# Kernel tuning notes

Hardware: AMD Instinct MI355X
Metric: run time of the kernel (lower is better)

## Reference

```python
import jax, jax.numpy as jnp
import numpy as np

B, LQ, LKV = 2, 2048, 1024
DQ = DK = DV_IN = 512
H, DQK, DV = 8, 64, 64
DOUT = 512
SPAN, STRIDE = 128, 2


def setup_inputs() -> dict:
    key = jax.random.key(0)
    ks = jax.random.split(key, 7)
    W_SCALE = 0.05  # keep pre-softmax logits in a sane range
    return {
        "q": jax.random.normal(ks[0], (B, LQ, DQ), jnp.float32),
        "k": jax.random.normal(ks[1], (B, LKV, DK), jnp.float32),
        "v": jax.random.normal(ks[2], (B, LKV, DV_IN), jnp.float32),
        "Wq": jax.random.normal(ks[3], (DQ, H * DQK), jnp.float32) * W_SCALE,
        "Wk": jax.random.normal(ks[4], (DK, H * DQK), jnp.float32) * W_SCALE,
        "Wv": jax.random.normal(ks[5], (DV_IN, H * DV), jnp.float32) * W_SCALE,
        "Wout": jax.random.normal(ks[6], (H * DV, DOUT), jnp.float32) * W_SCALE,
        "head_num": H,
        "span": SPAN,
        "stride": STRIDE,
    }


def reference(q, k, v, Wq, Wk, Wv, Wout, head_num, span, stride):
    batch, length_q, _ = q.shape
    length_kv = k.shape[1]
    width = -(-span // stride)  # ceil(span / stride)
    hd_qk = Wq.shape[1] // head_num
    hd_v = Wv.shape[1] // head_num

    Q = (q @ Wq).reshape(batch, length_q, head_num, hd_qk)
    K = (k @ Wk).reshape(batch, length_kv, head_num, hd_qk)
    V = (v @ Wv).reshape(batch, length_kv, head_num, hd_v)

    # Local-window indices: query j attends kv position j//stride + w - (width-1)
    j = jnp.arange(length_q)[:, None]            # [Lq, 1]
    w = jnp.arange(width)[None, :]               # [1, width]
    orig_col = w - (width - 1) + j // stride     # [Lq, width]
    valid = (orig_col >= 0) & (orig_col < length_kv) & \
            ((j % stride) <= span - 1 - (width - w - 1) * stride)
    mask = jnp.where(valid, 0.0, -jnp.inf).astype(q.dtype)
    idx = jnp.clip(orig_col, 0, length_kv - 1)   # masked entries are dont-care

    Kg = K[:, idx]                               # [B, Lq, width, H, dQK]
    # NOTE: original module applies NO 1/sqrt(d) scaling
    scores = jnp.einsum('bjhd,bjwhd->bhjw', Q, Kg) + mask[None, None]
    p = jax.nn.softmax(scores, axis=-1)          # [B, H, Lq, width]

    Vg = V[:, idx]                               # [B, Lq, width, H, dV]
    out = jnp.einsum('bhjw,bjwhd->bjhd', p, Vg)
    out = out.reshape(batch, length_q, head_num * hd_v)
    return out @ Wout
```

## Files before the change

### kernel.cpp

```cpp
#include <hip/hip_runtime.h>
#include <stdint.h>

typedef __bf16 bf16;
typedef __bf16 bf16x8 __attribute__((ext_vector_type(8)));
typedef float f32x4 __attribute__((ext_vector_type(4)));

#define NB    2
#define LQn   2048
#define LKVn  1024
#define DM    512
#define NH    8
#define HD    64

static __device__ __forceinline__ f32x4 mfma_bf16(bf16x8 a, bf16x8 b, f32x4 c) {
  return __builtin_amdgcn_mfma_f32_16x16x32_bf16(a, b, c, 0, 0, 0);
}

__global__ __launch_bounds__(256) void transpose_w_kernel(
    const float* __restrict__ Wq, const float* __restrict__ Wk,
    const float* __restrict__ Wv, const float* __restrict__ Wo,
    bf16* __restrict__ WThi) {
  __shared__ float tile[64 * 65];
  const int bid = blockIdx.x;
  const int mat = bid >> 6;
  const int tb  = bid & 63;
  const int r0 = (tb >> 3) * 64;
  const int c0 = (tb & 7) * 64;
  const float* W = (mat == 0) ? Wq : (mat == 1) ? Wk : (mat == 2) ? Wv : Wo;
  const int t = threadIdx.x;
#pragma unroll
  for (int i = 0; i < 16; ++i) {
    int idx = i * 256 + t;
    int r = idx >> 6, c = idx & 63;
    tile[r * 65 + c] = W[(size_t)(r0 + r) * DM + c0 + c];
  }
  __syncthreads();
#pragma unroll
  for (int i = 0; i < 16; ++i) {
    int idx = i * 256 + t;
    int r = idx >> 6, c = idx & 63;
    WThi[(size_t)mat * DM * DM + (size_t)(c0 + r) * DM + r0 + c] =
        (bf16)tile[c * 65 + r];
  }
}

template <bool SPLIT>
__device__ __forceinline__ void proj_tile(const float* __restrict__ Ap,
                                          const bf16* __restrict__ Bp,
                                          bf16* __restrict__ Chi,
                                          bf16* __restrict__ Clo,
                                          int m0, int n0,
                                          bf16* smAh, bf16* smAl, bf16* smBh) {
  const int t = threadIdx.x;
  const int lane = t & 63;
  const int w = t >> 6;
  const int ln = lane & 15, hi4 = lane >> 4;
  const int wr = w >> 2, wc = w & 3;
  const f32x4 zf = {0.f, 0.f, 0.f, 0.f};
  f32x4 acc[4][2];
#pragma unroll
  for (int a = 0; a < 4; ++a)
#pragma unroll
    for (int b = 0; b < 2; ++b) acc[a][b] = zf;

  for (int k0 = 0; k0 < 512; k0 += 64) {
    bf16x8 ahv[2], alv[2], bv[2];
#pragma unroll
    for (int i = 0; i < 2; ++i) {
      int idx = i * 512 + t;
      int r = idx >> 3, u = idx & 7;
      const float* g = Ap + (size_t)(m0 + r) * 512 + k0 + u * 8;
      f32x4 x0 = *(const f32x4*)g, x1 = *(const f32x4*)(g + 4);
      bf16x8 hv, lv;
#pragma unroll
      for (int e = 0; e < 4; ++e) {
        float x = x0[e]; bf16 hh = (bf16)x; hv[e] = hh;
        float y = x1[e]; bf16 h2 = (bf16)y; hv[4 + e] = h2;
        if constexpr (SPLIT) { lv[e] = (bf16)(x - (float)hh); lv[4 + e] = (bf16)(y - (float)h2); }
      }
      ahv[i] = hv; alv[i] = lv;
      bv[i] = *(const bf16x8*)(Bp + (size_t)(n0 + r) * 512 + k0 + u * 8);
    }
    __syncthreads();
#pragma unroll
    for (int i = 0; i < 2; ++i) {
      int idx = i * 512 + t;
      int r = idx >> 3, u = idx & 7;
      int sw = r * 64 + ((u ^ (r & 7)) * 8);
      *(bf16x8*)&smAh[sw] = ahv[i];
      if constexpr (SPLIT) *(bf16x8*)&smAl[sw] = alv[i];
      *(bf16x8*)&smBh[sw] = bv[i];
    }
    __syncthreads();
#pragma unroll
    for (int kk = 0; kk < 64; kk += 32) {
      const int ub = kk >> 3;
      bf16x8 ah[4], al[4], bh[2];
#pragma unroll
      for (int mf = 0; mf < 4; ++mf) {
        int row = wr * 64 + mf * 16 + ln;
        int addr = row * 64 + (((ub + hi4) ^ (ln & 7)) * 8);
        ah[mf] = *(const bf16x8*)&smAh[addr];
        if constexpr (SPLIT) al[mf] = *(const bf16x8*)&smAl[addr];
      }
#pragma unroll
      for (int nf = 0; nf < 2; ++nf) {
        int row = wc * 32 + nf * 16 + ln;
        int addr = row * 64 + (((ub + hi4) ^ (ln & 7)) * 8);
        bh[nf] = *(const bf16x8*)&smBh[addr];
      }
#pragma unroll
      for (int mf = 0; mf < 4; ++mf)
#pragma unroll
        for (int nf = 0; nf < 2; ++nf) {
          acc[mf][nf] = mfma_bf16(ah[mf], bh[nf], acc[mf][nf]);
          if constexpr (SPLIT) acc[mf][nf] = mfma_bf16(al[mf], bh[nf], acc[mf][nf]);
        }
    }
  }
#pragma unroll
  for (int mf = 0; mf < 4; ++mf)
#pragma unroll
    for (int nf = 0; nf < 2; ++nf)
#pragma unroll
      for (int e = 0; e < 4; ++e) {
        size_t off = (size_t)(m0 + wr * 64 + mf * 16 + hi4 * 4 + e) * 512 +
                     n0 + wc * 32 + nf * 16 + ln;
        float x = acc[mf][nf][e];
        bf16 h = (bf16)x;
        Chi[off] = h;
        if constexpr (SPLIT) Clo[off] = (bf16)(x - (float)h);
      }
}

__global__ __launch_bounds__(512, 2) void proj_kernel(
    const float* __restrict__ q, const float* __restrict__ k,
    const float* __restrict__ v, const bf16* __restrict__ WThi,
    bf16* __restrict__ Qhi, bf16* __restrict__ Qlo,
    bf16* __restrict__ Khi, bf16* __restrict__ Klo, bf16* __restrict__ Vb) {
  __shared__ bf16 smAh[128 * 64];
  __shared__ bf16 smAl[128 * 64];
  __shared__ bf16 smBh[128 * 64];
  const int bid = blockIdx.x;
  if (bid < 128) {
    int m0 = (bid >> 2) * 128, n0 = (bid & 3) * 128;
    proj_tile<true>(q, WThi, Qhi, Qlo, m0, n0, smAh, smAl, smBh);
  } else if (bid < 192) {
    int b2 = bid - 128;
    int m0 = (b2 >> 2) * 128, n0 = (b2 & 3) * 128;
    proj_tile<true>(k, WThi + (size_t)DM * DM, Khi, Klo, m0, n0, smAh, smAl, smBh);
  } else {
    int b2 = bid - 192;
    int m0 = (b2 >> 2) * 128, n0 = (b2 & 3) * 128;
    proj_tile<false>(v, WThi + (size_t)2 * DM * DM, Vb, nullptr, m0, n0,
                     smAh, smAl, smBh);
  }
}

__global__ __launch_bounds__(256) void outproj_kernel(
    const bf16* __restrict__ AO, const bf16* __restrict__ Bo,
    float* __restrict__ out) {
  __shared__ bf16 smA[64 * 64];
  __shared__ bf16 smB[128 * 64];
  const int bid = blockIdx.x;
  const int m0 = (bid >> 2) * 64, n0 = (bid & 3) * 128;
  const int t = threadIdx.x;
  const int lane = t & 63;
  const int w = t >> 6;
  const int ln = lane & 15, hi4 = lane >> 4;
  const f32x4 zf = {0.f, 0.f, 0.f, 0.f};
  f32x4 acc[4][2];
#pragma unroll
  for (int a = 0; a < 4; ++a)
#pragma unroll
    for (int b = 0; b < 2; ++b) acc[a][b] = zf;

  for (int k0 = 0; k0 < 512; k0 += 64) {
    bf16x8 av[2], bv[4];
#pragma unroll
    for (int i = 0; i < 2; ++i) {
      int idx = i * 256 + t;
      int r = idx >> 3, u = idx & 7;
      av[i] = *(const bf16x8*)(AO + (size_t)(m0 + r) * 512 + k0 + u * 8);
    }
#pragma unroll
    for (int i = 0; i < 4; ++i) {
      int idx = i * 256 + t;
      int r = idx >> 3, u = idx & 7;
      bv[i] = *(const bf16x8*)(Bo + (size_t)(n0 + r) * 512 + k0 + u * 8);
    }
    __syncthreads();
#pragma unroll
    for (int i = 0; i < 2; ++i) {
      int idx = i * 256 + t;
      int r = idx >> 3, u = idx & 7;
      *(bf16x8*)&smA[r * 64 + ((u ^ (r & 7)) * 8)] = av[i];
    }
#pragma unroll
    for (int i = 0; i < 4; ++i) {
      int idx = i * 256 + t;
      int r = idx >> 3, u = idx & 7;
      *(bf16x8*)&smB[r * 64 + ((u ^ (r & 7)) * 8)] = bv[i];
    }
    __syncthreads();
#pragma unroll
    for (int kk = 0; kk < 64; kk += 32) {
      const int ub = kk >> 3;
      bf16x8 af[4], bh[2];
#pragma unroll
      for (int mf = 0; mf < 4; ++mf) {
        int row = mf * 16 + ln;
        af[mf] = *(const bf16x8*)&smA[row * 64 + (((ub + hi4) ^ (ln & 7)) * 8)];
      }
#pragma unroll
      for (int nf = 0; nf < 2; ++nf) {
        int row = w * 32 + nf * 16 + ln;
        bh[nf] = *(const bf16x8*)&smB[row * 64 + (((ub + hi4) ^ (ln & 7)) * 8)];
      }
#pragma unroll
      for (int mf = 0; mf < 4; ++mf)
#pragma unroll
        for (int nf = 0; nf < 2; ++nf)
          acc[mf][nf] = mfma_bf16(af[mf], bh[nf], acc[mf][nf]);
    }
  }
#pragma unroll
  for (int mf = 0; mf < 4; ++mf)
#pragma unroll
    for (int nf = 0; nf < 2; ++nf)
#pragma unroll
      for (int e = 0; e < 4; ++e)
        out[(size_t)(m0 + mf * 16 + hi4 * 4 + e) * 512 +
            n0 + w * 32 + nf * 16 + ln] = acc[mf][nf][e];
}

__global__ __launch_bounds__(512, 2) void attn_kernel(
    const bf16* __restrict__ Qhi, const bf16* __restrict__ Qlo,
    const bf16* __restrict__ Khi, const bf16* __restrict__ Klo,
    const bf16* __restrict__ Vb, bf16* __restrict__ AO) {
  __shared__ bf16 smQh[128 * 64];
  __shared__ bf16 smQl[128 * 64];
  __shared__ bf16 smKh[128 * 64];
  __shared__ bf16 smKl[128 * 64];
  __shared__ bf16 smVt[64 * 128];
  __shared__ bf16 smP[128 * 128];
  const int bid = blockIdx.x;
  const int qt = bid & 15;
  const int h  = (bid >> 4) & 7;
  const int b  = bid >> 7;
  const int j0 = qt * 128;
  const int pbase = (j0 >> 1) - 63;
  const int t = threadIdx.x;
  const int lane = t & 63, w = t >> 6;
  const int ln = lane & 15, hi4 = lane >> 4;

#pragma unroll
  for (int i = 0; i < 2; ++i) {
    int idx = i * 512 + t;
    int r = idx >> 3, u = idx & 7;
    int sw = r * 64 + ((u ^ (r & 7)) * 8);
    size_t qoff = ((size_t)(b * LQn + j0 + r)) * 512 + h * 64 + u * 8;
    *(bf16x8*)&smQh[sw] = *(const bf16x8*)(Qhi + qoff);
    *(bf16x8*)&smQl[sw] = *(const bf16x8*)(Qlo + qoff);
    int p = pbase + r;
    p = p < 0 ? 0 : (p > LKVn - 1 ? LKVn - 1 : p);
    size_t koff = ((size_t)(b * LKVn + p)) * 512 + h * 64 + u * 8;
    *(bf16x8*)&smKh[sw] = *(const bf16x8*)(Khi + koff);
    *(bf16x8*)&smKl[sw] = *(const bf16x8*)(Klo + koff);
    bf16x8 vv = *(const bf16x8*)(Vb + koff);
#pragma unroll
    for (int e = 0; e < 8; ++e) {
      int rv = u * 8 + e;
      smVt[rv * 128 + (((r >> 3) ^ (rv & 15)) * 8) + (r & 7)] = vv[e];
    }
  }
  __syncthreads();

  const f32x4 zf = {0.f, 0.f, 0.f, 0.f};
  f32x4 s[8];
#pragma unroll
  for (int cf = 0; cf < 8; ++cf) s[cf] = zf;
#pragma unroll
  for (int kk = 0; kk < 64; kk += 32) {
    const int ub = kk >> 3;
    int rowq = w * 16 + ln;
    int addrq = rowq * 64 + (((ub + hi4) ^ (ln & 7)) * 8);
    bf16x8 ah = *(const bf16x8*)&smQh[addrq];
    bf16x8 al = *(const bf16x8*)&smQl[addrq];
#pragma unroll
    for (int cf = 0; cf < 8; ++cf) {
      int rowk = cf * 16 + ln;
      int addrk = rowk * 64 + (((ub + hi4) ^ (ln & 7)) * 8);
      bf16x8 bh = *(const bf16x8*)&smKh[addrk];
      bf16x8 bl = *(const bf16x8*)&smKl[addrk];
      s[cf] = mfma_bf16(ah, bh, s[cf]);
      s[cf] = mfma_bf16(ah, bl, s[cf]);
      s[cf] = mfma_bf16(al, bh, s[cf]);
    }
  }

#pragma unroll
  for (int r = 0; r < 4; ++r) {
    int rloc = w * 16 + hi4 * 4 + r;
    int wlo = rloc >> 1;
    int colmin = wlo > -pbase ? wlo : -pbase;
    int colmax = wlo + 63;
    float sv[8];
    float mx = -1e30f;
#pragma unroll
    for (int cf = 0; cf < 8; ++cf) {
      int col = cf * 16 + ln;
      float val = s[cf][r];
      bool ok = (col >= colmin) && (col <= colmax);
      sv[cf] = ok ? val : -1e30f;
      mx = fmaxf(mx, sv[cf]);
    }
#pragma unroll
    for (int msk = 1; msk < 16; msk <<= 1) mx = fmaxf(mx, __shfl_xor(mx, msk, 64));
    float sum = 0.f;
#pragma unroll
    for (int cf = 0; cf < 8; ++cf) {
      sv[cf] = __expf(sv[cf] - mx);
      sum += sv[cf];
    }
#pragma unroll
    for (int msk = 1; msk < 16; msk <<= 1) sum += __shfl_xor(sum, msk, 64);
    float rs = 1.0f / sum;
#pragma unroll
    for (int cf = 0; cf < 8; ++cf) {
      int uu = cf * 2 + (ln >> 3);
      smP[rloc * 128 + ((uu ^ (rloc & 15)) * 8) + (ln & 7)] = (bf16)(sv[cf] * rs);
    }
  }
  __syncthreads();

  f32x4 o[4];
#pragma unroll
  for (int nf = 0; nf < 4; ++nf) o[nf] = zf;
#pragma unroll
  for (int kk = 0; kk < 128; kk += 32) {
    const int ub = kk >> 3;
    int rowp = w * 16 + ln;
    bf16x8 pa = *(const bf16x8*)&smP[rowp * 128 + (((ub + hi4) ^ ln) * 8)];
#pragma unroll
    for (int nf = 0; nf < 4; ++nf) {
      int d = nf * 16 + ln;
      bf16x8 vf = *(const bf16x8*)&smVt[d * 128 + (((ub + hi4) ^ ln) * 8)];
      o[nf] = mfma_bf16(pa, vf, o[nf]);
    }
  }

#pragma unroll
  for (int nf = 0; nf < 4; ++nf)
#pragma unroll
    for (int e = 0; e < 4; ++e) {
      int rloc = w * 16 + hi4 * 4 + e;
      AO[((size_t)(b * LQn + j0 + rloc)) * 512 + h * 64 + nf * 16 + ln] =
          (bf16)o[nf][e];
    }
}

extern "C" void kernel_launch(void* const* d_in, const int* in_sizes, int n_in,
                              void* d_out, int out_size, void* d_ws, size_t ws_size,
                              hipStream_t stream) {
  const float* q    = (const float*)d_in[0];
  const float* k    = (const float*)d_in[1];
  const float* v    = (const float*)d_in[2];
  const float* Wq   = (const float*)d_in[3];
  const float* Wk   = (const float*)d_in[4];
  const float* Wv   = (const float*)d_in[5];
  const float* Wout = (const float*)d_in[6];
  float* out = (float*)d_out;

  char* ws = (char*)d_ws;
  bf16* WThi = (bf16*)ws;
  bf16* Qhi  = (bf16*)(ws + (size_t)(2  << 20));
  bf16* Qlo  = (bf16*)(ws + (size_t)(6  << 20));
  bf16* Khi  = (bf16*)(ws + (size_t)(10 << 20));
  bf16* Klo  = (bf16*)(ws + (size_t)(12 << 20));
  bf16* Vbuf = (bf16*)(ws + (size_t)(14 << 20));
  bf16* AO   = (bf16*)(ws + (size_t)(16 << 20));

  transpose_w_kernel<<<256, 256, 0, stream>>>(Wq, Wk, Wv, Wout, WThi);
  proj_kernel<<<256, 512, 0, stream>>>(q, k, v, WThi, Qhi, Qlo, Khi, Klo, Vbuf);
  attn_kernel<<<256, 512, 0, stream>>>(Qhi, Qlo, Khi, Klo, Vbuf, AO);
  outproj_kernel<<<256, 256, 0, stream>>>(AO, WThi + (size_t)3 * DM * DM, out);
}
```

Baseline: 46.03 us.

## Pre-swizzle global layouts and use direct global-to-LDS loads with double buffering

Weights, Q/K projections and attention output are now written to global memory already in the XOR-swizzled LDS layout. The GEMM and attention kernels can then load tiles with global_load_lds (direct global-to-LDS DMA) instead of going through registers. The projection and output-projection GEMMs are double-buffered so the next k-tile's loads overlap the current MFMAs, and block IDs are remapped across XCDs for locality. This aims to cut register staging and load latency, but it ties every kernel to the swizzled layout and enlarges LDS use, which could lower occupancy.

```diff
diff --git a/kernel.cpp b/kernel.cpp
--- a/kernel.cpp
+++ b/kernel.cpp
@@ -5,21 +5,26 @@
 typedef __bf16 bf16x8 __attribute__((ext_vector_type(8)));
 typedef float f32x4 __attribute__((ext_vector_type(4)));
 
-#define NB    2
 #define LQn   2048
 #define LKVn  1024
 #define DM    512
 #define NH    8
-#define HD    64
 
 static __device__ __forceinline__ f32x4 mfma_bf16(bf16x8 a, bf16x8 b, f32x4 c) {
   return __builtin_amdgcn_mfma_f32_16x16x32_bf16(a, b, c, 0, 0, 0);
 }
+
+static __device__ __forceinline__ void gl_lds16(const void* g, void* l) {
+  __builtin_amdgcn_global_load_lds(
+      (const __attribute__((address_space(1))) void*)g,
+      (__attribute__((address_space(3))) void*)l, 16, 0, 0);
+}
+
 
 __global__ __launch_bounds__(256) void transpose_w_kernel(
     const float* __restrict__ Wq, const float* __restrict__ Wk,
     const float* __restrict__ Wv, const float* __restrict__ Wo,
-    bf16* __restrict__ WThi) {
+    bf16* __restrict__ WTs) {
   __shared__ float tile[64 * 65];
   const int bid = blockIdx.x;
   const int mat = bid >> 6;
@@ -39,23 +44,25 @@
   for (int i = 0; i < 16; ++i) {
     int idx = i * 256 + t;
     int r = idx >> 6, c = idx & 63;
-    WThi[(size_t)mat * DM * DM + (size_t)(c0 + r) * DM + r0 + c] =
-        (bf16)tile[c * 65 + r];
-  }
-}
-
-template <bool SPLIT>
+    int n = c0 + r, k = r0 + c;
+    int ks = (k & ~63) | ((((k >> 3) & 7) ^ (n & 7)) << 3) | (k & 7);
+    WTs[(size_t)mat * DM * DM + (size_t)n * DM + ks] = (bf16)tile[c * 65 + r];
+  }
+}
+
+template <bool SPLIT, bool SWZ_OUT>
 __device__ __forceinline__ void proj_tile(const float* __restrict__ Ap,
-                                          const bf16* __restrict__ Bp,
+                                          const bf16* __restrict__ Bs,
                                           bf16* __restrict__ Chi,
                                           bf16* __restrict__ Clo,
                                           int m0, int n0,
-                                          bf16* smAh, bf16* smAl, bf16* smBh) {
+                                          bf16* smAh, bf16* smAl, bf16* smB) {
   const int t = threadIdx.x;
   const int lane = t & 63;
   const int w = t >> 6;
   const int ln = lane & 15, hi4 = lane >> 4;
   const int wr = w >> 2, wc = w & 3;
+  const int rS = t >> 3, uS = t & 7;
   const f32x4 zf = {0.f, 0.f, 0.f, 0.f};
   f32x4 acc[4][2];
 #pragma unroll
@@ -63,13 +70,19 @@
 #pragma unroll
     for (int b = 0; b < 2; ++b) acc[a][b] = zf;
 
-  for (int k0 = 0; k0 < 512; k0 += 64) {
-    bf16x8 ahv[2], alv[2], bv[2];
+  bf16x8 ahv[2], alv[2], nahv[2], nalv[2];
+
+  auto issueB = [&](int ko, int buf) {
 #pragma unroll
     for (int i = 0; i < 2; ++i) {
-      int idx = i * 512 + t;
-      int r = idx >> 3, u = idx & 7;
-      const float* g = Ap + (size_t)(m0 + r) * 512 + k0 + u * 8;
+      const bf16* src = Bs + (size_t)(n0 + i * 64 + rS) * 512 + ko + uS * 8;
+      gl_lds16(src, smB + buf * 8192 + i * 4096 + w * 512);
+    }
+  };
+  auto loadA = [&](int ko, bf16x8* hv8, bf16x8* lv8) {
+#pragma unroll
+    for (int i = 0; i < 2; ++i) {
+      const float* g = Ap + (size_t)(m0 + i * 64 + rS) * 512 + ko + uS * 8;
       f32x4 x0 = *(const f32x4*)g, x1 = *(const f32x4*)(g + 4);
       bf16x8 hv, lv;
 #pragma unroll
@@ -78,36 +91,45 @@
         float y = x1[e]; bf16 h2 = (bf16)y; hv[4 + e] = h2;
         if constexpr (SPLIT) { lv[e] = (bf16)(x - (float)hh); lv[4 + e] = (bf16)(y - (float)h2); }
       }
-      ahv[i] = hv; alv[i] = lv;
-      bv[i] = *(const bf16x8*)(Bp + (size_t)(n0 + r) * 512 + k0 + u * 8);
-    }
-    __syncthreads();
+      hv8[i] = hv; lv8[i] = lv;
+    }
+  };
+  auto writeA = [&](bf16x8* hv8, bf16x8* lv8) {
 #pragma unroll
     for (int i = 0; i < 2; ++i) {
-      int idx = i * 512 + t;
-      int r = idx >> 3, u = idx & 7;
-      int sw = r * 64 + ((u ^ (r & 7)) * 8);
-      *(bf16x8*)&smAh[sw] = ahv[i];
-      if constexpr (SPLIT) *(bf16x8*)&smAl[sw] = alv[i];
-      *(bf16x8*)&smBh[sw] = bv[i];
-    }
-    __syncthreads();
+      int r = i * 64 + rS;
+      int sw = r * 64 + ((uS ^ (r & 7)) * 8);
+      *(bf16x8*)&smAh[sw] = hv8[i];
+      if constexpr (SPLIT) *(bf16x8*)&smAl[sw] = lv8[i];
+    }
+  };
+
+  issueB(0, 0);
+  loadA(0, ahv, alv);
+  writeA(ahv, alv);
+  __syncthreads();
+
+  int buf = 0;
+  for (int kt = 0; kt < 8; ++kt) {
+    if (kt < 7) {
+      issueB((kt + 1) * 64, buf ^ 1);
+      loadA((kt + 1) * 64, nahv, nalv);
+    }
 #pragma unroll
     for (int kk = 0; kk < 64; kk += 32) {
       const int ub = kk >> 3;
       bf16x8 ah[4], al[4], bh[2];
 #pragma unroll
       for (int mf = 0; mf < 4; ++mf) {
-        int row = wr * 64 + mf * 16 + ln;
-        int addr = row * 64 + (((ub + hi4) ^ (ln & 7)) * 8);
+        int addr = (wr * 64 + mf * 16 + ln) * 64 + (((ub + hi4) ^ (ln & 7)) * 8);
         ah[mf] = *(const bf16x8*)&smAh[addr];
         if constexpr (SPLIT) al[mf] = *(const bf16x8*)&smAl[addr];
       }
 #pragma unroll
       for (int nf = 0; nf < 2; ++nf) {
-        int row = wc * 32 + nf * 16 + ln;
-        int addr = row * 64 + (((ub + hi4) ^ (ln & 7)) * 8);
-        bh[nf] = *(const bf16x8*)&smBh[addr];
+        int addr = buf * 8192 + (wc * 32 + nf * 16 + ln) * 64 +
+                   (((ub + hi4) ^ (ln & 7)) * 8);
+        bh[nf] = *(const bf16x8*)&smB[addr];
       }
 #pragma unroll
       for (int mf = 0; mf < 4; ++mf)
@@ -117,6 +139,12 @@
           if constexpr (SPLIT) acc[mf][nf] = mfma_bf16(al[mf], bh[nf], acc[mf][nf]);
         }
     }
+    if (kt < 7) {
+      __syncthreads();
+      writeA(nahv, nalv);
+      __syncthreads();
+      buf ^= 1;
+    }
   }
 #pragma unroll
   for (int mf = 0; mf < 4; ++mf)
@@ -124,8 +152,11 @@
     for (int nf = 0; nf < 2; ++nf)
 #pragma unroll
       for (int e = 0; e < 4; ++e) {
-        size_t off = (size_t)(m0 + wr * 64 + mf * 16 + hi4 * 4 + e) * 512 +
-                     n0 + wc * 32 + nf * 16 + ln;
+        int row = m0 + wr * 64 + mf * 16 + hi4 * 4 + e;
+        int col = n0 + wc * 32 + nf * 16 + ln;
+        if constexpr (SWZ_OUT)
+          col = (col & ~63) | ((((col >> 3) & 7) ^ (row & 7)) << 3) | (col & 7);
+        size_t off = (size_t)row * 512 + col;
         float x = acc[mf][nf][e];
         bf16 h = (bf16)x;
         Chi[off] = h;
@@ -135,39 +166,41 @@
 
 __global__ __launch_bounds__(512, 2) void proj_kernel(
     const float* __restrict__ q, const float* __restrict__ k,
-    const float* __restrict__ v, const bf16* __restrict__ WThi,
+    const float* __restrict__ v, const bf16* __restrict__ WTs,
     bf16* __restrict__ Qhi, bf16* __restrict__ Qlo,
     bf16* __restrict__ Khi, bf16* __restrict__ Klo, bf16* __restrict__ Vb) {
   __shared__ bf16 smAh[128 * 64];
   __shared__ bf16 smAl[128 * 64];
-  __shared__ bf16 smBh[128 * 64];
-  const int bid = blockIdx.x;
+  __shared__ bf16 smB[2 * 128 * 64];
+  const int bid = ((blockIdx.x & 7) << 5) | (blockIdx.x >> 3);
   if (bid < 128) {
     int m0 = (bid >> 2) * 128, n0 = (bid & 3) * 128;
-    proj_tile<true>(q, WThi, Qhi, Qlo, m0, n0, smAh, smAl, smBh);
+    proj_tile<true, true>(q, WTs, Qhi, Qlo, m0, n0, smAh, smAl, smB);
   } else if (bid < 192) {
     int b2 = bid - 128;
     int m0 = (b2 >> 2) * 128, n0 = (b2 & 3) * 128;
-    proj_tile<true>(k, WThi + (size_t)DM * DM, Khi, Klo, m0, n0, smAh, smAl, smBh);
+    proj_tile<true, true>(k, WTs + (size_t)DM * DM, Khi, Klo, m0, n0,
+                          smAh, smAl, smB);
   } else {
     int b2 = bid - 192;
     int m0 = (b2 >> 2) * 128, n0 = (b2 & 3) * 128;
-    proj_tile<false>(v, WThi + (size_t)2 * DM * DM, Vb, nullptr, m0, n0,
-                     smAh, smAl, smBh);
+    proj_tile<false, false>(v, WTs + (size_t)2 * DM * DM, Vb, nullptr, m0, n0,
+                            smAh, smAl, smB);
   }
 }
 
 __global__ __launch_bounds__(256) void outproj_kernel(
     const bf16* __restrict__ AO, const bf16* __restrict__ Bo,
     float* __restrict__ out) {
-  __shared__ bf16 smA[64 * 64];
-  __shared__ bf16 smB[128 * 64];
-  const int bid = blockIdx.x;
+  __shared__ bf16 smA[2 * 64 * 64];
+  __shared__ bf16 smB[2 * 128 * 64];
+  const int bid = ((blockIdx.x & 7) << 5) | (blockIdx.x >> 3);
   const int m0 = (bid >> 2) * 64, n0 = (bid & 3) * 128;
   const int t = threadIdx.x;
   const int lane = t & 63;
   const int w = t >> 6;
   const int ln = lane & 15, hi4 = lane >> 4;
+  const int rS = t >> 3, uS = t & 7;
   const f32x4 zf = {0.f, 0.f, 0.f, 0.f};
   f32x4 acc[4][2];
 #pragma unroll
@@ -175,54 +208,44 @@
 #pragma unroll
     for (int b = 0; b < 2; ++b) acc[a][b] = zf;
 
-  for (int k0 = 0; k0 < 512; k0 += 64) {
-    bf16x8 av[2], bv[4];
+  auto issueAB = [&](int ko, int buf) {
 #pragma unroll
     for (int i = 0; i < 2; ++i) {
-      int idx = i * 256 + t;
-      int r = idx >> 3, u = idx & 7;
-      av[i] = *(const bf16x8*)(AO + (size_t)(m0 + r) * 512 + k0 + u * 8);
+      const bf16* src = AO + (size_t)(m0 + i * 32 + rS) * 512 + ko + uS * 8;
+      gl_lds16(src, smA + buf * 4096 + i * 2048 + w * 512);
     }
 #pragma unroll
     for (int i = 0; i < 4; ++i) {
-      int idx = i * 256 + t;
-      int r = idx >> 3, u = idx & 7;
-      bv[i] = *(const bf16x8*)(Bo + (size_t)(n0 + r) * 512 + k0 + u * 8);
-    }
-    __syncthreads();
-#pragma unroll
-    for (int i = 0; i < 2; ++i) {
-      int idx = i * 256 + t;
-      int r = idx >> 3, u = idx & 7;
-      *(bf16x8*)&smA[r * 64 + ((u ^ (r & 7)) * 8)] = av[i];
-    }
-#pragma unroll
-    for (int i = 0; i < 4; ++i) {
-      int idx = i * 256 + t;
-      int r = idx >> 3, u = idx & 7;
-      *(bf16x8*)&smB[r * 64 + ((u ^ (r & 7)) * 8)] = bv[i];
-    }
-    __syncthreads();
+      const bf16* src = Bo + (size_t)(n0 + i * 32 + rS) * 512 + ko + uS * 8;
+      gl_lds16(src, smB + buf * 8192 + i * 2048 + w * 512);
+    }
+  };
+
+  issueAB(0, 0);
+  __syncthreads();
+  int buf = 0;
+  for (int kt = 0; kt < 8; ++kt) {
+    if (kt < 7) issueAB((kt + 1) * 64, buf ^ 1);
 #pragma unroll
     for (int kk = 0; kk < 64; kk += 32) {
       const int ub = kk >> 3;
       bf16x8 af[4], bh[2];
 #pragma unroll
-      for (int mf = 0; mf < 4; ++mf) {
-        int row = mf * 16 + ln;
-        af[mf] = *(const bf16x8*)&smA[row * 64 + (((ub + hi4) ^ (ln & 7)) * 8)];
-      }
-#pragma unroll
-      for (int nf = 0; nf < 2; ++nf) {
-        int row = w * 32 + nf * 16 + ln;
-        bh[nf] = *(const bf16x8*)&smB[row * 64 + (((ub + hi4) ^ (ln & 7)) * 8)];
-      }
+      for (int mf = 0; mf < 4; ++mf)
+        af[mf] = *(const bf16x8*)&smA[buf * 4096 + (mf * 16 + ln) * 64 +
+                                      (((ub + hi4) ^ (ln & 7)) * 8)];
+#pragma unroll
+      for (int nf = 0; nf < 2; ++nf)
+        bh[nf] = *(const bf16x8*)&smB[buf * 8192 + (w * 32 + nf * 16 + ln) * 64 +
+                                      (((ub + hi4) ^ (ln & 7)) * 8)];
 #pragma unroll
       for (int mf = 0; mf < 4; ++mf)
 #pragma unroll
         for (int nf = 0; nf < 2; ++nf)
           acc[mf][nf] = mfma_bf16(af[mf], bh[nf], acc[mf][nf]);
     }
+    __syncthreads();
+    buf ^= 1;
   }
 #pragma unroll
   for (int mf = 0; mf < 4; ++mf)
@@ -244,7 +267,7 @@
   __shared__ bf16 smKl[128 * 64];
   __shared__ bf16 smVt[64 * 128];
   __shared__ bf16 smP[128 * 128];
-  const int bid = blockIdx.x;
+  const int bid = ((blockIdx.x & 7) << 5) | (blockIdx.x >> 3);
   const int qt = bid & 15;
   const int h  = (bid >> 4) & 7;
   const int b  = bid >> 7;
@@ -253,24 +276,23 @@
   const int t = threadIdx.x;
   const int lane = t & 63, w = t >> 6;
   const int ln = lane & 15, hi4 = lane >> 4;
+  const int rS = t >> 3, uS = t & 7;
 
 #pragma unroll
   for (int i = 0; i < 2; ++i) {
-    int idx = i * 512 + t;
-    int r = idx >> 3, u = idx & 7;
-    int sw = r * 64 + ((u ^ (r & 7)) * 8);
-    size_t qoff = ((size_t)(b * LQn + j0 + r)) * 512 + h * 64 + u * 8;
-    *(bf16x8*)&smQh[sw] = *(const bf16x8*)(Qhi + qoff);
-    *(bf16x8*)&smQl[sw] = *(const bf16x8*)(Qlo + qoff);
+    int r = i * 64 + rS;
+    size_t qoff = ((size_t)(b * LQn + j0 + r)) * 512 + h * 64 + uS * 8;
+    gl_lds16(Qhi + qoff, smQh + i * 4096 + w * 512);
+    gl_lds16(Qlo + qoff, smQl + i * 4096 + w * 512);
     int p = pbase + r;
     p = p < 0 ? 0 : (p > LKVn - 1 ? LKVn - 1 : p);
-    size_t koff = ((size_t)(b * LKVn + p)) * 512 + h * 64 + u * 8;
-    *(bf16x8*)&smKh[sw] = *(const bf16x8*)(Khi + koff);
-    *(bf16x8*)&smKl[sw] = *(const bf16x8*)(Klo + koff);
+    size_t koff = ((size_t)(b * LKVn + p)) * 512 + h * 64 + uS * 8;
+    gl_lds16(Khi + koff, smKh + i * 4096 + w * 512);
+    gl_lds16(Klo + koff, smKl + i * 4096 + w * 512);
     bf16x8 vv = *(const bf16x8*)(Vb + koff);
 #pragma unroll
     for (int e = 0; e < 8; ++e) {
-      int rv = u * 8 + e;
+      int rv = uS * 8 + e;
       smVt[rv * 128 + (((r >> 3) ^ (rv & 15)) * 8) + (r & 7)] = vv[e];
     }
   }
@@ -283,14 +305,12 @@
 #pragma unroll
   for (int kk = 0; kk < 64; kk += 32) {
     const int ub = kk >> 3;
-    int rowq = w * 16 + ln;
-    int addrq = rowq * 64 + (((ub + hi4) ^ (ln & 7)) * 8);
+    int addrq = (w * 16 + ln) * 64 + (((ub + hi4) ^ (ln & 7)) * 8);
     bf16x8 ah = *(const bf16x8*)&smQh[addrq];
     bf16x8 al = *(const bf16x8*)&smQl[addrq];
 #pragma unroll
     for (int cf = 0; cf < 8; ++cf) {
-      int rowk = cf * 16 + ln;
-      int addrk = rowk * 64 + (((ub + hi4) ^ (ln & 7)) * 8);
+      int addrk = (cf * 16 + ln) * 64 + (((ub + hi4) ^ ((ln + 1) & 7)) * 8);
       bf16x8 bh = *(const bf16x8*)&smKh[addrk];
       bf16x8 bl = *(const bf16x8*)&smKl[addrk];
       s[cf] = mfma_bf16(ah, bh, s[cf]);
@@ -340,8 +360,7 @@
 #pragma unroll
   for (int kk = 0; kk < 128; kk += 32) {
     const int ub = kk >> 3;
-    int rowp = w * 16 + ln;
-    bf16x8 pa = *(const bf16x8*)&smP[rowp * 128 + (((ub + hi4) ^ ln) * 8)];
+    bf16x8 pa = *(const bf16x8*)&smP[(w * 16 + ln) * 128 + (((ub + hi4) ^ ln) * 8)];
 #pragma unroll
     for (int nf = 0; nf < 4; ++nf) {
       int d = nf * 16 + ln;
@@ -355,8 +374,9 @@
 #pragma unroll
     for (int e = 0; e < 4; ++e) {
       int rloc = w * 16 + hi4 * 4 + e;
-      AO[((size_t)(b * LQn + j0 + rloc)) * 512 + h * 64 + nf * 16 + ln] =
-          (bf16)o[nf][e];
+      int u3 = nf * 2 + (ln >> 3);
+      int col = h * 64 + ((u3 ^ (rloc & 7)) << 3) + (ln & 7);
+      AO[((size_t)(b * LQn + j0 + rloc)) * 512 + col] = (bf16)o[nf][e];
     }
 }
 
@@ -373,7 +393,7 @@
   float* out = (float*)d_out;
 
   char* ws = (char*)d_ws;
-  bf16* WThi = (bf16*)ws;
+  bf16* WTs  = (bf16*)ws;
   bf16* Qhi  = (bf16*)(ws + (size_t)(2  << 20));
   bf16* Qlo  = (bf16*)(ws + (size_t)(6  << 20));
   bf16* Khi  = (bf16*)(ws + (size_t)(10 << 20));
@@ -381,8 +401,8 @@
   bf16* Vbuf = (bf16*)(ws + (size_t)(14 << 20));
   bf16* AO   = (bf16*)(ws + (size_t)(16 << 20));
 
-  transpose_w_kernel<<<256, 256, 0, stream>>>(Wq, Wk, Wv, Wout, WThi);
-  proj_kernel<<<256, 512, 0, stream>>>(q, k, v, WThi, Qhi, Qlo, Khi, Klo, Vbuf);
+  transpose_w_kernel<<<256, 256, 0, stream>>>(Wq, Wk, Wv, Wout, WTs);
+  proj_kernel<<<256, 512, 0, stream>>>(q, k, v, WTs, Qhi, Qlo, Khi, Klo, Vbuf);
   attn_kernel<<<256, 512, 0, stream>>>(Qhi, Qlo, Khi, Klo, Vbuf, AO);
-  outproj_kernel<<<256, 256, 0, stream>>>(AO, WThi + (size_t)3 * DM * DM, out);
-}
+  outproj_kernel<<<256, 256, 0, stream>>>(AO, WTs + (size_t)3 * DM * DM, out);
+}
```

Measured after the change: 46.50 us. No clear change (+1.0%).

## Drop weight transpose kernel; read fp32 weights directly into MFMA B fragments

Applied to the files above, without the earlier changes.

Removes the separate transpose/convert kernel for the weights. The projection and output-projection GEMMs now load fp32 weights straight from global memory with strided per-element gathers and convert them in registers. The projection kernel also double-buffers the A tile in LDS to overlap the next load with compute, and the output projection drops LDS staging entirely. This saves one launch and the weight round-trip, but the strided uncoalesced weight loads and repeated per-block conversion may cost more memory traffic.

```diff
diff --git a/kernel.cpp b/kernel.cpp
--- a/kernel.cpp
+++ b/kernel.cpp
@@ -5,52 +5,22 @@
 typedef __bf16 bf16x8 __attribute__((ext_vector_type(8)));
 typedef float f32x4 __attribute__((ext_vector_type(4)));
 
-#define NB    2
 #define LQn   2048
 #define LKVn  1024
 #define DM    512
 #define NH    8
-#define HD    64
 
 static __device__ __forceinline__ f32x4 mfma_bf16(bf16x8 a, bf16x8 b, f32x4 c) {
   return __builtin_amdgcn_mfma_f32_16x16x32_bf16(a, b, c, 0, 0, 0);
 }
 
-__global__ __launch_bounds__(256) void transpose_w_kernel(
-    const float* __restrict__ Wq, const float* __restrict__ Wk,
-    const float* __restrict__ Wv, const float* __restrict__ Wo,
-    bf16* __restrict__ WThi) {
-  __shared__ float tile[64 * 65];
-  const int bid = blockIdx.x;
-  const int mat = bid >> 6;
-  const int tb  = bid & 63;
-  const int r0 = (tb >> 3) * 64;
-  const int c0 = (tb & 7) * 64;
-  const float* W = (mat == 0) ? Wq : (mat == 1) ? Wk : (mat == 2) ? Wv : Wo;
-  const int t = threadIdx.x;
-#pragma unroll
-  for (int i = 0; i < 16; ++i) {
-    int idx = i * 256 + t;
-    int r = idx >> 6, c = idx & 63;
-    tile[r * 65 + c] = W[(size_t)(r0 + r) * DM + c0 + c];
-  }
-  __syncthreads();
-#pragma unroll
-  for (int i = 0; i < 16; ++i) {
-    int idx = i * 256 + t;
-    int r = idx >> 6, c = idx & 63;
-    WThi[(size_t)mat * DM * DM + (size_t)(c0 + r) * DM + r0 + c] =
-        (bf16)tile[c * 65 + r];
-  }
-}
-
 template <bool SPLIT>
-__device__ __forceinline__ void proj_tile(const float* __restrict__ Ap,
-                                          const bf16* __restrict__ Bp,
-                                          bf16* __restrict__ Chi,
-                                          bf16* __restrict__ Clo,
-                                          int m0, int n0,
-                                          bf16* smAh, bf16* smAl, bf16* smBh) {
+__device__ __forceinline__ void proj_tile2(const float* __restrict__ Ap,
+                                           const float* __restrict__ Wp,
+                                           bf16* __restrict__ Chi,
+                                           bf16* __restrict__ Clo,
+                                           int m0, int n0,
+                                           bf16* smAh, bf16* smAl) {
   const int t = threadIdx.x;
   const int lane = t & 63;
   const int w = t >> 6;
@@ -63,13 +33,12 @@
 #pragma unroll
     for (int b = 0; b < 2; ++b) acc[a][b] = zf;
 
-  for (int k0 = 0; k0 < 512; k0 += 64) {
-    bf16x8 ahv[2], alv[2], bv[2];
+  auto loadA = [&](int ko, bf16x8* hv8, bf16x8* lv8) {
 #pragma unroll
     for (int i = 0; i < 2; ++i) {
       int idx = i * 512 + t;
       int r = idx >> 3, u = idx & 7;
-      const float* g = Ap + (size_t)(m0 + r) * 512 + k0 + u * 8;
+      const float* g = Ap + (size_t)(m0 + r) * 512 + ko + u * 8;
       f32x4 x0 = *(const f32x4*)g, x1 = *(const f32x4*)(g + 4);
       bf16x8 hv, lv;
 #pragma unroll
@@ -78,44 +47,66 @@
         float y = x1[e]; bf16 h2 = (bf16)y; hv[4 + e] = h2;
         if constexpr (SPLIT) { lv[e] = (bf16)(x - (float)hh); lv[4 + e] = (bf16)(y - (float)h2); }
       }
-      ahv[i] = hv; alv[i] = lv;
-      bv[i] = *(const bf16x8*)(Bp + (size_t)(n0 + r) * 512 + k0 + u * 8);
-    }
-    __syncthreads();
+      hv8[i] = hv; lv8[i] = lv;
+    }
+  };
+  auto writeA = [&](int buf, bf16x8* hv8, bf16x8* lv8) {
 #pragma unroll
     for (int i = 0; i < 2; ++i) {
       int idx = i * 512 + t;
       int r = idx >> 3, u = idx & 7;
-      int sw = r * 64 + ((u ^ (r & 7)) * 8);
-      *(bf16x8*)&smAh[sw] = ahv[i];
-      if constexpr (SPLIT) *(bf16x8*)&smAl[sw] = alv[i];
-      *(bf16x8*)&smBh[sw] = bv[i];
-    }
-    __syncthreads();
-#pragma unroll
-    for (int kk = 0; kk < 64; kk += 32) {
-      const int ub = kk >> 3;
-      bf16x8 ah[4], al[4], bh[2];
+      int sw = buf * 8192 + r * 64 + ((u ^ (r & 7)) * 8);
+      *(bf16x8*)&smAh[sw] = hv8[i];
+      if constexpr (SPLIT) *(bf16x8*)&smAl[sw] = lv8[i];
+    }
+  };
+  auto bfrag = [&](int kbase, int nf) {
+    int n = n0 + wc * 32 + nf * 16 + ln;
+    const float* gp = Wp + (size_t)kbase * 512 + n;
+    bf16x8 r;
+#pragma unroll
+    for (int e = 0; e < 8; ++e) r[e] = (bf16)gp[(size_t)e * 512];
+    return r;
+  };
+
+  bf16x8 cah[2], cal[2];
+  loadA(0, cah, cal);
+  writeA(0, cah, cal);
+  __syncthreads();
+
+  int cur = 0;
+  for (int kt = 0; kt < 8; ++kt) {
+    bf16x8 nah[2], nal[2];
+    if (kt < 7) loadA((kt + 1) * 64, nah, nal);
+    bf16x8 bh[2][2];
+#pragma unroll
+    for (int kk2 = 0; kk2 < 2; ++kk2)
+#pragma unroll
+      for (int nf = 0; nf < 2; ++nf)
+        bh[kk2][nf] = bfrag(kt * 64 + kk2 * 32 + hi4 * 8, nf);
+#pragma unroll
+    for (int kk2 = 0; kk2 < 2; ++kk2) {
+      const int ub = kk2 * 4;
+      bf16x8 ah[4], al[4];
 #pragma unroll
       for (int mf = 0; mf < 4; ++mf) {
-        int row = wr * 64 + mf * 16 + ln;
-        int addr = row * 64 + (((ub + hi4) ^ (ln & 7)) * 8);
+        int addr = cur * 8192 + (wr * 64 + mf * 16 + ln) * 64 +
+                   (((ub + hi4) ^ (ln & 7)) * 8);
         ah[mf] = *(const bf16x8*)&smAh[addr];
         if constexpr (SPLIT) al[mf] = *(const bf16x8*)&smAl[addr];
       }
 #pragma unroll
-      for (int nf = 0; nf < 2; ++nf) {
-        int row = wc * 32 + nf * 16 + ln;
-        int addr = row * 64 + (((ub + hi4) ^ (ln & 7)) * 8);
-        bh[nf] = *(const bf16x8*)&smBh[addr];
-      }
-#pragma unroll
       for (int mf = 0; mf < 4; ++mf)
 #pragma unroll
         for (int nf = 0; nf < 2; ++nf) {
-          acc[mf][nf] = mfma_bf16(ah[mf], bh[nf], acc[mf][nf]);
-          if constexpr (SPLIT) acc[mf][nf] = mfma_bf16(al[mf], bh[nf], acc[mf][nf]);
+          acc[mf][nf] = mfma_bf16(ah[mf], bh[kk2][nf], acc[mf][nf]);
+          if constexpr (SPLIT) acc[mf][nf] = mfma_bf16(al[mf], bh[kk2][nf], acc[mf][nf]);
         }
+    }
+    if (kt < 7) {
+      writeA(cur ^ 1, nah, nal);
+      __syncthreads();
+      cur ^= 1;
     }
   }
 #pragma unroll
@@ -135,33 +126,30 @@
 
 __global__ __launch_bounds__(512, 2) void proj_kernel(
     const float* __restrict__ q, const float* __restrict__ k,
-    const float* __restrict__ v, const bf16* __restrict__ WThi,
+    const float* __restrict__ v, const float* __restrict__ Wq,
+    const float* __restrict__ Wk, const float* __restrict__ Wv,
     bf16* __restrict__ Qhi, bf16* __restrict__ Qlo,
     bf16* __restrict__ Khi, bf16* __restrict__ Klo, bf16* __restrict__ Vb) {
-  __shared__ bf16 smAh[128 * 64];
-  __shared__ bf16 smAl[128 * 64];
-  __shared__ bf16 smBh[128 * 64];
+  __shared__ bf16 smAh[2 * 128 * 64];
+  __shared__ bf16 smAl[2 * 128 * 64];
   const int bid = blockIdx.x;
   if (bid < 128) {
     int m0 = (bid >> 2) * 128, n0 = (bid & 3) * 128;
-    proj_tile<true>(q, WThi, Qhi, Qlo, m0, n0, smAh, smAl, smBh);
+    proj_tile2<true>(q, Wq, Qhi, Qlo, m0, n0, smAh, smAl);
   } else if (bid < 192) {
     int b2 = bid - 128;
     int m0 = (b2 >> 2) * 128, n0 = (b2 & 3) * 128;
-    proj_tile<true>(k, WThi + (size_t)DM * DM, Khi, Klo, m0, n0, smAh, smAl, smBh);
+    proj_tile2<true>(k, Wk, Khi, Klo, m0, n0, smAh, smAl);
   } else {
     int b2 = bid - 192;
     int m0 = (b2 >> 2) * 128, n0 = (b2 & 3) * 128;
-    proj_tile<false>(v, WThi + (size_t)2 * DM * DM, Vb, nullptr, m0, n0,
-                     smAh, smAl, smBh);
+    proj_tile2<false>(v, Wv, Vb, nullptr, m0, n0, smAh, smAl);
   }
 }
 
 __global__ __launch_bounds__(256) void outproj_kernel(
-    const bf16* __restrict__ AO, const bf16* __restrict__ Bo,
+    const bf16* __restrict__ AO, const float* __restrict__ Wo,
     float* __restrict__ out) {
-  __shared__ bf16 smA[64 * 64];
-  __shared__ bf16 smB[128 * 64];
   const int bid = blockIdx.x;
   const int m0 = (bid >> 2) * 64, n0 = (bid & 3) * 128;
   const int t = threadIdx.x;
@@ -175,47 +163,20 @@
 #pragma unroll
     for (int b = 0; b < 2; ++b) acc[a][b] = zf;
 
-  for (int k0 = 0; k0 < 512; k0 += 64) {
-    bf16x8 av[2], bv[4];
-#pragma unroll
-    for (int i = 0; i < 2; ++i) {
-      int idx = i * 256 + t;
-      int r = idx >> 3, u = idx & 7;
-      av[i] = *(const bf16x8*)(AO + (size_t)(m0 + r) * 512 + k0 + u * 8);
-    }
-#pragma unroll
-    for (int i = 0; i < 4; ++i) {
-      int idx = i * 256 + t;
-      int r = idx >> 3, u = idx & 7;
-      bv[i] = *(const bf16x8*)(Bo + (size_t)(n0 + r) * 512 + k0 + u * 8);
-    }
-    __syncthreads();
-#pragma unroll
-    for (int i = 0; i < 2; ++i) {
-      int idx = i * 256 + t;
-      int r = idx >> 3, u = idx & 7;
-      *(bf16x8*)&smA[r * 64 + ((u ^ (r & 7)) * 8)] = av[i];
-    }
-#pragma unroll
-    for (int i = 0; i < 4; ++i) {
-      int idx = i * 256 + t;
-      int r = idx >> 3, u = idx & 7;
-      *(bf16x8*)&smB[r * 64 + ((u ^ (r & 7)) * 8)] = bv[i];
-    }
-    __syncthreads();
-#pragma unroll
-    for (int kk = 0; kk < 64; kk += 32) {
-      const int ub = kk >> 3;
+  for (int kt = 0; kt < 8; ++kt) {
+#pragma unroll
+    for (int kk2 = 0; kk2 < 2; ++kk2) {
+      const int kb = kt * 64 + kk2 * 32 + hi4 * 8;
       bf16x8 af[4], bh[2];
 #pragma unroll
-      for (int mf = 0; mf < 4; ++mf) {
-        int row = mf * 16 + ln;
-        af[mf] = *(const bf16x8*)&smA[row * 64 + (((ub + hi4) ^ (ln & 7)) * 8)];
-      }
+      for (int mf = 0; mf < 4; ++mf)
+        af[mf] = *(const bf16x8*)(AO + (size_t)(m0 + mf * 16 + ln) * 512 + kb);
 #pragma unroll
       for (int nf = 0; nf < 2; ++nf) {
-        int row = w * 32 + nf * 16 + ln;
-        bh[nf] = *(const bf16x8*)&smB[row * 64 + (((ub + hi4) ^ (ln & 7)) * 8)];
+        int n = n0 + w * 32 + nf * 16 + ln;
+        const float* gp = Wo + (size_t)kb * 512 + n;
+#pragma unroll
+        for (int e = 0; e < 8; ++e) bh[nf][e] = (bf16)gp[(size_t)e * 512];
       }
 #pragma unroll
       for (int mf = 0; mf < 4; ++mf)
@@ -283,14 +244,12 @@
 #pragma unroll
   for (int kk = 0; kk < 64; kk += 32) {
     const int ub = kk >> 3;
-    int rowq = w * 16 + ln;
-    int addrq = rowq * 64 + (((ub + hi4) ^ (ln & 7)) * 8);
+    int addrq = (w * 16 + ln) * 64 + (((ub + hi4) ^ (ln & 7)) * 8);
     bf16x8 ah = *(const bf16x8*)&smQh[addrq];
     bf16x8 al = *(const bf16x8*)&smQl[addrq];
 #pragma unroll
     for (int cf = 0; cf < 8; ++cf) {
-      int rowk = cf * 16 + ln;
-      int addrk = rowk * 64 + (((ub + hi4) ^ (ln & 7)) * 8);
+      int addrk = (cf * 16 + ln) * 64 + (((ub + hi4) ^ (ln & 7)) * 8);
       bf16x8 bh = *(const bf16x8*)&smKh[addrk];
       bf16x8 bl = *(const bf16x8*)&smKl[addrk];
       s[cf] = mfma_bf16(ah, bh, s[cf]);
@@ -340,8 +299,7 @@
 #pragma unroll
   for (int kk = 0; kk < 128; kk += 32) {
     const int ub = kk >> 3;
-    int rowp = w * 16 + ln;
-    bf16x8 pa = *(const bf16x8*)&smP[rowp * 128 + (((ub + hi4) ^ ln) * 8)];
+    bf16x8 pa = *(const bf16x8*)&smP[(w * 16 + ln) * 128 + (((ub + hi4) ^ ln) * 8)];
 #pragma unroll
     for (int nf = 0; nf < 4; ++nf) {
       int d = nf * 16 + ln;
@@ -373,16 +331,15 @@
   float* out = (float*)d_out;
 
   char* ws = (char*)d_ws;
-  bf16* WThi = (bf16*)ws;
-  bf16* Qhi  = (bf16*)(ws + (size_t)(2  << 20));
-  bf16* Qlo  = (bf16*)(ws + (size_t)(6  << 20));
-  bf16* Khi  = (bf16*)(ws + (size_t)(10 << 20));
-  bf16* Klo  = (bf16*)(ws + (size_t)(12 << 20));
-  bf16* Vbuf = (bf16*)(ws + (size_t)(14 << 20));
-  bf16* AO   = (bf16*)(ws + (size_t)(16 << 20));
-
-  transpose_w_kernel<<<256, 256, 0, stream>>>(Wq, Wk, Wv, Wout, WThi);
-  proj_kernel<<<256, 512, 0, stream>>>(q, k, v, WThi, Qhi, Qlo, Khi, Klo, Vbuf);
+  bf16* Qhi  = (bf16*)ws;
+  bf16* Qlo  = (bf16*)(ws + (size_t)(4  << 20));
+  bf16* Khi  = (bf16*)(ws + (size_t)(8  << 20));
+  bf16* Klo  = (bf16*)(ws + (size_t)(10 << 20));
+  bf16* Vbuf = (bf16*)(ws + (size_t)(12 << 20));
+  bf16* AO   = (bf16*)(ws + (size_t)(14 << 20));
+
+  proj_kernel<<<256, 512, 0, stream>>>(q, k, v, Wq, Wk, Wv,
+                                       Qhi, Qlo, Khi, Klo, Vbuf);
   attn_kernel<<<256, 512, 0, stream>>>(Qhi, Qlo, Khi, Klo, Vbuf, AO);
-  outproj_kernel<<<256, 256, 0, stream>>>(AO, WThi + (size_t)3 * DM * DM, out);
-}
+  outproj_kernel<<<256, 256, 0, stream>>>(AO, Wout, out);
+}
```

Result: slower. 51.18 us (+11.2%).
